# Performance work log

Hardware: AMD Instinct MI355X
Metric: run time of the kernel (lower is better)

## Reference

```python
import jax, jax.numpy as jnp
import numpy as np

N = 200000   # nodes
E = 600000   # edges
D = 128      # input_channels
H = 128      # hidden_channels
EPS = 1e-5   # BatchNorm1d eps


def setup_inputs() -> dict:
    key = jax.random.key(0)
    ks = jax.random.split(key, 6)
    x = jax.random.normal(ks[0], (N, D), dtype=jnp.float32)
    edge_index = jax.random.randint(ks[1], (2, E), 0, N)
    a1 = jnp.full((1,), 0.25, dtype=jnp.float32)   # PReLU init
    gamma = jnp.ones((D,), dtype=jnp.float32)
    beta = jnp.zeros((D,), dtype=jnp.float32)
    W1 = jax.random.normal(ks[2], (D, H), dtype=jnp.float32) / np.float32(np.sqrt(D))
    b1 = jnp.zeros((H,), dtype=jnp.float32)
    a2 = jnp.full((1,), 0.25, dtype=jnp.float32)
    W2 = jax.random.normal(ks[3], (H, D), dtype=jnp.float32) / np.float32(np.sqrt(H))
    b2 = jnp.zeros((D,), dtype=jnp.float32)
    return dict(x=x, edge_index=edge_index, a1=a1, gamma=gamma, beta=beta,
                W1=W1, b1=b1, a2=a2, W2=W2, b2=b2)


def _prelu(x, a):
    return jnp.where(x >= 0, x, a[0] * x)


def _batchnorm(x, gamma, beta):
    # training-mode BatchNorm1d: batch mean, biased variance
    mean = jnp.mean(x, axis=0)
    var = jnp.mean(jnp.square(x - mean), axis=0)
    return (x - mean) * jax.lax.rsqrt(var + EPS) * gamma + beta


def _gcn_conv(x, W, b, src, dst, n):
    # PyG GCNConv: add self-loops, symmetric normalization D^-1/2 (A+I) D^-1/2
    h = x @ W                                            # [n, out]
    deg = jnp.ones((n,), h.dtype).at[dst].add(1.0)       # degree incl. self-loop
    dinv = jax.lax.rsqrt(deg)
    coef = (dinv[src] * dinv[dst])[:, None]              # [E, 1]
    msg = h[src] * coef                                  # gather  [E, out]
    out = jax.ops.segment_sum(msg, dst, num_segments=n)  # scatter [n, out]
    out = out + h * (1.0 / deg)[:, None]                 # self-loop term
    return out + b


def reference(x, edge_index, a1, gamma, beta, W1, b1, a2, W2, b2):
    src, dst = edge_index[0], edge_index[1]
    n = x.shape[0]
    h = _prelu(x, a1)
    h = _batchnorm(h, gamma, beta)
    h = _gcn_conv(h, W1, b1, src, dst, n)
    h = _prelu(h, a2)
    h = _gcn_conv(h, W2, b2, src, dst, n)
    return h
```

## Files before the change

kernel.cpp:

```cpp
#include <hip/hip_runtime.h>

#define NN 200000
#define NE 600000
#define DD 128
#define GT 1563

constexpr float BN_EPS = 1e-5f;

typedef unsigned short u16;
typedef short bf16x8 __attribute__((ext_vector_type(8)));
typedef float f32x4  __attribute__((ext_vector_type(4)));
typedef float f32x2  __attribute__((ext_vector_type(2)));


__global__ void k_zero(int* __restrict__ cnt, float* __restrict__ ssum, float* __restrict__ ssq) {
  int i = blockIdx.x*256 + threadIdx.x;
  if (i < NN) cnt[i] = 0;
  if (i < DD) { ssum[i] = 0.f; ssq[i] = 0.f; }
}

__global__ void k_count(const int* __restrict__ ei, int* __restrict__ cnt) {
  int e = blockIdx.x*256 + threadIdx.x;
  if (e < NE) atomicAdd(&cnt[ei[NE + e]], 1);
}

__global__ void k_stats(const float* __restrict__ x, const float* __restrict__ a1p,
                        float* __restrict__ ssum, float* __restrict__ ssq) {
  __shared__ float s1[8][128], s2[8][128];
  const int c4 = (threadIdx.x & 31) * 4;
  const int rg = threadIdx.x >> 5;
  float a1 = *a1p;
  float acc1[4] = {0.f,0.f,0.f,0.f}, acc2[4] = {0.f,0.f,0.f,0.f};
  const int stride = gridDim.x * 8;
  for (int r = blockIdx.x*8 + rg; r < NN; r += stride) {
    float4 v = *(const float4*)(x + (size_t)r*DD + c4);
    float vv[4] = {v.x, v.y, v.z, v.w};
    #pragma unroll
    for (int i = 0; i < 4; ++i) {
      float u = vv[i];
      u = (u >= 0.f) ? u : a1*u;
      acc1[i] += u; acc2[i] += u*u;
    }
  }
  *(float4*)&s1[rg][c4] = make_float4(acc1[0], acc1[1], acc1[2], acc1[3]);
  *(float4*)&s2[rg][c4] = make_float4(acc2[0], acc2[1], acc2[2], acc2[3]);
  __syncthreads();
  if (threadIdx.x < 128) {
    int col = threadIdx.x;
    float t1 = 0.f, t2 = 0.f;
    #pragma unroll
    for (int g = 0; g < 8; ++g) { t1 += s1[g][col]; t2 += s2[g][col]; }
    atomicAdd(&ssum[col], t1);
    atomicAdd(&ssq [col], t2);
  }
}

__global__ void k_bn_tw1(const float* __restrict__ ssum, const float* __restrict__ ssq,
                         const float* __restrict__ gamma, const float* __restrict__ beta,
                         const float* __restrict__ W1,
                         float* __restrict__ sarr, float* __restrict__ tarr,
                         float* __restrict__ tw1) {
  __shared__ float ts[128];
  int j = threadIdx.x;
  float mean = ssum[j] * (1.f/NN);
  float var  = ssq[j] * (1.f/NN) - mean*mean;
  float s = gamma[j] * rsqrtf(var + BN_EPS);
  float t = beta[j] - mean*s;
  sarr[j] = s; tarr[j] = t; ts[j] = t;
  __syncthreads();
  float acc = 0.f;
  #pragma unroll 8
  for (int k = 0; k < 128; ++k) acc += ts[k] * W1[k*DD + j];
  tw1[j] = acc;
}

__global__ void k_wprep(const float* __restrict__ W, const float* __restrict__ s,
                        u16* __restrict__ hi, u16* __restrict__ lo) {
  int idx = blockIdx.x*256 + threadIdx.x;
  int j = idx >> 7, k = idx & 127;
  float v = W[(size_t)k*DD + j];
  if (s) v *= s[k];
  unsigned hb = __float_as_uint(v) & 0xffff0000u;
  float r = v - __uint_as_float(hb);
  hi[idx] = (u16)(hb >> 16);
  lo[idx] = (u16)(__float_as_uint(r) >> 16);
}


__global__ void k_scan1(const int* __restrict__ cnt, int* __restrict__ rp, int* __restrict__ bsums) {
  __shared__ int sm[256];
  int tid = threadIdx.x;
  int base = blockIdx.x*1024 + tid*4;
  int4 v = make_int4(0,0,0,0);
  if (base + 3 < NN) v = *(const int4*)(cnt + base);
  else {
    if (base   < NN) v.x = cnt[base];
    if (base+1 < NN) v.y = cnt[base+1];
    if (base+2 < NN) v.z = cnt[base+2];
    if (base+3 < NN) v.w = cnt[base+3];
  }
  int p1 = v.x, p2 = p1 + v.y, p3 = p2 + v.z, tsum = p3 + v.w;
  sm[tid] = tsum; __syncthreads();
  for (int off = 1; off < 256; off <<= 1) {
    int t = (tid >= off) ? sm[tid - off] : 0; __syncthreads();
    sm[tid] += t; __syncthreads();
  }
  int inc = sm[tid];
  int excl = inc - tsum;
  if (base   < NN) rp[base]   = excl;
  if (base+1 < NN) rp[base+1] = excl + p1;
  if (base+2 < NN) rp[base+2] = excl + p2;
  if (base+3 < NN) rp[base+3] = excl + p3;
  if (tid == 255) bsums[blockIdx.x] = inc;
}

__global__ void k_scan2(int* __restrict__ bsums, int nb) {
  __shared__ int sm[256];
  int tid = threadIdx.x;
  int v = (tid < nb) ? bsums[tid] : 0;
  sm[tid] = v; __syncthreads();
  for (int off = 1; off < 256; off <<= 1) {
    int t = (tid >= off) ? sm[tid - off] : 0; __syncthreads();
    sm[tid] += t; __syncthreads();
  }
  if (tid < nb) bsums[tid] = sm[tid] - v;
}

__global__ void k_scan3(int* __restrict__ rp, const int* __restrict__ bsums,
                        int* __restrict__ cur, const int* __restrict__ cnt,
                        float* __restrict__ dinv) {
  int i = blockIdx.x*256 + threadIdx.x;
  if (i < NN) {
    int val = rp[i] + bsums[i >> 10];
    rp[i] = val; cur[i] = val;
    dinv[i] = rsqrtf((float)(cnt[i] + 1));
  }
  if (i == 0) rp[NN] = NE;
}

__global__ void k_fill(const int* __restrict__ ei, const float* __restrict__ dinv,
                       int* __restrict__ cur, int2* __restrict__ pairs) {
  int e = blockIdx.x*256 + threadIdx.x;
  if (e < NE) {
    int s = ei[e], d = ei[NE + e];
    int pos = atomicAdd(&cur[d], 1);
    float cf = dinv[s] * dinv[d];
    pairs[pos] = make_int2(s, __float_as_int(cf));
  }
}


template<bool FUSE, bool ADDROW>
__global__ __launch_bounds__(256)
void k_gemm(const float* __restrict__ A,
            const u16* __restrict__ wt_hi, const u16* __restrict__ wt_lo,
            float* __restrict__ C,
            const float* __restrict__ tw1, const float* __restrict__ a1p)
{
  __shared__ u16 Bh[128][136];
  __shared__ u16 Bl[128][136];
  const int tid = threadIdx.x;

  #pragma unroll
  for (int i = 0; i < 8; ++i) {
    int c = tid + i*256;
    int row = c >> 4, slot = c & 15;
    *(uint4*)&Bh[row][slot*8] = ((const uint4*)wt_hi)[c];
    *(uint4*)&Bl[row][slot*8] = ((const uint4*)wt_lo)[c];
  }

  float a1v = 0.f;
  if constexpr (FUSE) a1v = *a1p;

  const int lane = tid & 63;
  const int wv   = tid >> 6;
  const int lr   = lane & 15;
  const int lk   = lane >> 4;
  const int r0   = blockIdx.x*128 + wv*32;

  f32x4 acc[2][8];
  #pragma unroll
  for (int s = 0; s < 2; ++s)
    #pragma unroll
    for (int j = 0; j < 8; ++j) acc[s][j] = (f32x4){0.f,0.f,0.f,0.f};

  __syncthreads();

  #pragma unroll
  for (int kc = 0; kc < 4; ++kc) {
    bf16x8 ah[2], al[2];
    #pragma unroll
    for (int s = 0; s < 2; ++s) {
      int r = r0 + s*16 + lr; r = (r < NN) ? r : (NN-1);
      const float* ap = A + (size_t)r*DD + kc*32 + lk*8;
      float4 v0 = *(const float4*)ap;
      float4 v1 = *(const float4*)(ap + 4);
      float vv[8] = {v0.x,v0.y,v0.z,v0.w,v1.x,v1.y,v1.z,v1.w};
      #pragma unroll
      for (int e = 0; e < 8; ++e) {
        float v = vv[e];
        if constexpr (FUSE) v = (v >= 0.f) ? v : a1v*v;
        unsigned hb = __float_as_uint(v) & 0xffff0000u;
        float rres = v - __uint_as_float(hb);
        ah[s][e] = (short)(hb >> 16);
        al[s][e] = (short)(__float_as_uint(rres) >> 16);
      }
    }
    #pragma unroll
    for (int j = 0; j < 8; ++j) {
      int wrow = j*16 + lr;
      bf16x8 bh = *(const bf16x8*)&Bh[wrow][kc*32 + lk*8];
      bf16x8 bl = *(const bf16x8*)&Bl[wrow][kc*32 + lk*8];
      #pragma unroll
      for (int s = 0; s < 2; ++s) {
        acc[s][j] = __builtin_amdgcn_mfma_f32_16x16x32_bf16(ah[s], bh, acc[s][j], 0, 0, 0);
        acc[s][j] = __builtin_amdgcn_mfma_f32_16x16x32_bf16(ah[s], bl, acc[s][j], 0, 0, 0);
        acc[s][j] = __builtin_amdgcn_mfma_f32_16x16x32_bf16(al[s], bh, acc[s][j], 0, 0, 0);
      }
    }
  }

  float tw[8];
  #pragma unroll
  for (int j = 0; j < 8; ++j) tw[j] = 0.f;
  if constexpr (ADDROW) {
    #pragma unroll
    for (int j = 0; j < 8; ++j) tw[j] = tw1[j*16 + lr];
  }

  #pragma unroll
  for (int s = 0; s < 2; ++s) {
    #pragma unroll
    for (int g = 0; g < 4; ++g) {
      int row = r0 + s*16 + lk*4 + g;
      if (row < NN) {
        float* cp = C + (size_t)row*DD + lr;
        #pragma unroll
        for (int j = 0; j < 8; ++j) cp[j*16] = acc[s][j][g] + tw[j];
      }
    }
  }
}


template<bool PRELU>
__global__ __launch_bounds__(256)
void k_agg(const float* __restrict__ h, const int* __restrict__ rp,
           const int2* __restrict__ pairs,
           const float* __restrict__ bias, const float* __restrict__ a2p,
           float* __restrict__ out)
{
  const int wave = threadIdx.x >> 6;
  const int lane = threadIdx.x & 63;
  const int nb = (blockIdx.x*4 + wave) * 8;
  if (nb >= NN) return;
  const float2* h2 = (const float2*)h;
  f32x2* o2 = (f32x2*)out;

  int rv = 0;
  if (lane < 9) rv = rp[nb + lane];
  int beg[8], cnt8[8];
  #pragma unroll
  for (int i = 0; i < 8; ++i) {
    int b0 = __builtin_amdgcn_readfirstlane(__shfl(rv, i));
    int b1 = __builtin_amdgcn_readfirstlane(__shfl(rv, i+1));
    beg[i] = b0; cnt8[i] = b1 - b0;
  }

  float2 b = ((const float2*)bias)[lane];
  float a2 = 1.f;
  if constexpr (PRELU) a2 = *a2p;

  float2 acc[8];
  #pragma unroll
  for (int i = 0; i < 8; ++i) {
    float2 self = h2[(size_t)(nb+i)*64 + lane];
    float sc = 1.f / (float)(cnt8[i] + 1);
    acc[i].x = sc*self.x + b.x;
    acc[i].y = sc*self.y + b.y;
  }

  int maxc = 0;
  #pragma unroll
  for (int i = 0; i < 8; ++i) maxc = max(maxc, cnt8[i]);

  for (int c = 0; c < maxc; ++c) {
    int2 p[8];
    #pragma unroll
    for (int i = 0; i < 8; ++i)
      if (c < cnt8[i]) p[i] = pairs[beg[i] + c];
    #pragma unroll
    for (int i = 0; i < 8; ++i)
      if (c < cnt8[i]) {
        float2 g = h2[(size_t)p[i].x*64 + lane];
        float cf = __int_as_float(p[i].y);
        acc[i].x += cf*g.x; acc[i].y += cf*g.y;
      }
  }

  #pragma unroll
  for (int i = 0; i < 8; ++i) {
    float ax = acc[i].x, ay = acc[i].y;
    if constexpr (PRELU) {
      ax = (ax >= 0.f) ? ax : a2*ax;
      ay = (ay >= 0.f) ? ay : a2*ay;
    }
    f32x2 o; o[0] = ax; o[1] = ay;
    __builtin_nontemporal_store(o, &o2[(size_t)(nb+i)*64 + lane]);
  }
}


extern "C" void kernel_launch(void* const* d_in, const int* in_sizes, int n_in,
                              void* d_out, int out_size, void* d_ws, size_t ws_size,
                              hipStream_t stream) {
  const float* x     = (const float*)d_in[0];
  const int*   ei    = (const int*)  d_in[1];
  const float* a1    = (const float*)d_in[2];
  const float* gamma = (const float*)d_in[3];
  const float* beta  = (const float*)d_in[4];
  const float* W1    = (const float*)d_in[5];
  const float* b1    = (const float*)d_in[6];
  const float* a2    = (const float*)d_in[7];
  const float* W2    = (const float*)d_in[8];
  const float* b2    = (const float*)d_in[9];
  float* out = (float*)d_out;

  char* w = (char*)d_ws;
  auto alloc = [&](size_t bytes) { char* p = w; w += (bytes + 255) & ~(size_t)255; return p; };
  float* hbuf  = (float*)alloc((size_t)NN*DD*4);
  float* dinv  = (float*)alloc((size_t)NN*4);
  int*   cnt   = (int*)  alloc((size_t)NN*4);
  int*   rp    = (int*)  alloc((size_t)(NN+1)*4);
  int*   cur   = (int*)  alloc((size_t)NN*4);
  int2*  pairs = (int2*) alloc((size_t)NE*8);
  int*   bsums = (int*)  alloc(256*4);
  float* ssum  = (float*)alloc(128*4);
  float* ssq   = (float*)alloc(128*4);
  float* sarr  = (float*)alloc(128*4);
  float* tarr  = (float*)alloc(128*4);
  float* tw1   = (float*)alloc(128*4);
  u16*   w1h   = (u16*)  alloc(128*128*2);
  u16*   w1l   = (u16*)  alloc(128*128*2);
  u16*   w2h   = (u16*)  alloc(128*128*2);
  u16*   w2l   = (u16*)  alloc(128*128*2);

  const int nblkN = (NN + 255)/256;
  const int nblkE = (NE + 255)/256;
  const int nblkA = NN/32;

  k_zero  <<<nblkN, 256, 0, stream>>>(cnt, ssum, ssq);
  k_count <<<nblkE, 256, 0, stream>>>(ei, cnt);
  k_stats <<<1024,  256, 0, stream>>>(x, a1, ssum, ssq);
  k_bn_tw1<<<1,     128, 0, stream>>>(ssum, ssq, gamma, beta, W1, sarr, tarr, tw1);
  k_wprep <<<64,    256, 0, stream>>>(W2, nullptr, w2h, w2l);
  k_wprep <<<64,    256, 0, stream>>>(W1, sarr,    w1h, w1l);
  k_scan1 <<<196,   256, 0, stream>>>(cnt, rp, bsums);
  k_scan2 <<<1,     256, 0, stream>>>(bsums, 196);
  k_scan3 <<<nblkN, 256, 0, stream>>>(rp, bsums, cur, cnt, dinv);
  k_fill  <<<nblkE, 256, 0, stream>>>(ei, dinv, cur, pairs);

  k_gemm<true,  true ><<<GT, 256, 0, stream>>>(x,   w1h, w1l, hbuf, tw1, a1);
  k_agg <true >        <<<nblkA, 256, 0, stream>>>(hbuf, rp, pairs, b1, a2, out);
  k_gemm<false, false><<<GT, 256, 0, stream>>>(out, w2h, w2l, hbuf, nullptr, nullptr);
  k_agg <false>        <<<nblkA, 256, 0, stream>>>(hbuf, rp, pairs, b2, nullptr, out);
}
```

Before: 515.9 us.

## Fuse first aggregation, PReLU and second GEMM into one kernel

Adds a kernel that aggregates neighbors for 32 nodes per block, applies bias and PReLU, splits the result into bf16 hi/lo parts in shared memory, and immediately multiplies by W2 with MFMA, writing the second-layer features to a new buffer. This removes one full N×128 fp32 write and read round-trip plus a separate GEMM launch. It needs an extra N×128 workspace buffer and falls back to the old path if the workspace is too small. W2 fragments are read straight from global memory in every block rather than staged.

After: 503.5 us. 2.4% less time.

```diff
diff --git a/kernel.cpp b/kernel.cpp
--- a/kernel.cpp
+++ b/kernel.cpp
@@ -240,6 +240,116 @@
       }
     }
   }
+}
+
+
+__global__ __launch_bounds__(256)
+void k_fagg(const float* __restrict__ h, const int* __restrict__ rp,
+            const int2* __restrict__ pairs,
+            const u16* __restrict__ w2h, const u16* __restrict__ w2l,
+            const float* __restrict__ b1, const float* __restrict__ a2p,
+            float* __restrict__ h2)
+{
+  __shared__ u16 Ghi[32][136];
+  __shared__ u16 Glo[32][136];
+  const int wave = threadIdx.x >> 6;
+  const int lane = threadIdx.x & 63;
+  const int nbB  = blockIdx.x * 32;
+  const int nb   = nbB + wave*8;
+  const float2* hv = (const float2*)h;
+
+  int rv = 0;
+  if (lane < 9) rv = rp[nb + lane];
+  int beg[8], cnt8[8];
+  #pragma unroll
+  for (int i = 0; i < 8; ++i) {
+    int b0 = __builtin_amdgcn_readfirstlane(__shfl(rv, i));
+    int b1v = __builtin_amdgcn_readfirstlane(__shfl(rv, i+1));
+    beg[i] = b0; cnt8[i] = b1v - b0;
+  }
+
+  float2 b = ((const float2*)b1)[lane];
+  float2 acc[8];
+  #pragma unroll
+  for (int i = 0; i < 8; ++i) {
+    float2 self = hv[(size_t)(nb+i)*64 + lane];
+    float sc = 1.f / (float)(cnt8[i] + 1);
+    acc[i].x = sc*self.x + b.x;
+    acc[i].y = sc*self.y + b.y;
+  }
+
+  int maxc = 0;
+  #pragma unroll
+  for (int i = 0; i < 8; ++i) maxc = max(maxc, cnt8[i]);
+
+  for (int c = 0; c < maxc; ++c) {
+    int2 p[8];
+    #pragma unroll
+    for (int i = 0; i < 8; ++i)
+      if (c < cnt8[i]) p[i] = pairs[beg[i] + c];
+    #pragma unroll
+    for (int i = 0; i < 8; ++i)
+      if (c < cnt8[i]) {
+        float2 g = hv[(size_t)p[i].x*64 + lane];
+        float cf = __int_as_float(p[i].y);
+        acc[i].x += cf*g.x; acc[i].y += cf*g.y;
+      }
+  }
+
+  float a2 = *a2p;
+  #pragma unroll
+  for (int i = 0; i < 8; ++i) {
+    float ax = acc[i].x, ay = acc[i].y;
+    ax = (ax >= 0.f) ? ax : a2*ax;
+    ay = (ay >= 0.f) ? ay : a2*ay;
+    unsigned hx = __float_as_uint(ax) & 0xffff0000u;
+    unsigned hy = __float_as_uint(ay) & 0xffff0000u;
+    float rx = ax - __uint_as_float(hx);
+    float ry = ay - __uint_as_float(hy);
+    unsigned hiw = (hx >> 16) | hy;
+    unsigned low = (__float_as_uint(rx) >> 16) | (__float_as_uint(ry) & 0xffff0000u);
+    int row = wave*8 + i;
+    *(unsigned*)&Ghi[row][lane*2] = hiw;
+    *(unsigned*)&Glo[row][lane*2] = low;
+  }
+  __syncthreads();
+
+  const int lr = lane & 15, lk = lane >> 4;
+  f32x4 dacc[2][2];
+  #pragma unroll
+  for (int s = 0; s < 2; ++s)
+    #pragma unroll
+    for (int t = 0; t < 2; ++t) dacc[s][t] = (f32x4){0.f,0.f,0.f,0.f};
+
+  #pragma unroll
+  for (int kc = 0; kc < 4; ++kc) {
+    bf16x8 ah0 = *(const bf16x8*)&Ghi[lr]   [kc*32 + lk*8];
+    bf16x8 al0 = *(const bf16x8*)&Glo[lr]   [kc*32 + lk*8];
+    bf16x8 ah1 = *(const bf16x8*)&Ghi[16+lr][kc*32 + lk*8];
+    bf16x8 al1 = *(const bf16x8*)&Glo[16+lr][kc*32 + lk*8];
+    #pragma unroll
+    for (int t = 0; t < 2; ++t) {
+      int wrow = wave*32 + t*16 + lr;
+      bf16x8 bh = *(const bf16x8*)(w2h + (size_t)wrow*DD + kc*32 + lk*8);
+      bf16x8 bl = *(const bf16x8*)(w2l + (size_t)wrow*DD + kc*32 + lk*8);
+      dacc[0][t] = __builtin_amdgcn_mfma_f32_16x16x32_bf16(ah0, bh, dacc[0][t], 0, 0, 0);
+      dacc[0][t] = __builtin_amdgcn_mfma_f32_16x16x32_bf16(ah0, bl, dacc[0][t], 0, 0, 0);
+      dacc[0][t] = __builtin_amdgcn_mfma_f32_16x16x32_bf16(al0, bh, dacc[0][t], 0, 0, 0);
+      dacc[1][t] = __builtin_amdgcn_mfma_f32_16x16x32_bf16(ah1, bh, dacc[1][t], 0, 0, 0);
+      dacc[1][t] = __builtin_amdgcn_mfma_f32_16x16x32_bf16(ah1, bl, dacc[1][t], 0, 0, 0);
+      dacc[1][t] = __builtin_amdgcn_mfma_f32_16x16x32_bf16(al1, bh, dacc[1][t], 0, 0, 0);
+    }
+  }
+
+  #pragma unroll
+  for (int s = 0; s < 2; ++s)
+    #pragma unroll
+    for (int t = 0; t < 2; ++t)
+      #pragma unroll
+      for (int g = 0; g < 4; ++g) {
+        int row = nbB + s*16 + lk*4 + g;
+        h2[(size_t)row*DD + wave*32 + t*16 + lr] = dacc[s][t][g];
+      }
 }
 
 
@@ -344,10 +454,13 @@
   u16*   w1l   = (u16*)  alloc(128*128*2);
   u16*   w2h   = (u16*)  alloc(128*128*2);
   u16*   w2l   = (u16*)  alloc(128*128*2);
+  float* hbuf2 = (float*)alloc((size_t)NN*DD*4);
+  const bool fused = ((size_t)(w - (char*)d_ws) <= ws_size);
 
   const int nblkN = (NN + 255)/256;
   const int nblkE = (NE + 255)/256;
   const int nblkA = NN/32;
+  const int nblkF = NN/32;
 
   k_zero  <<<nblkN, 256, 0, stream>>>(cnt, ssum, ssq);
   k_count <<<nblkE, 256, 0, stream>>>(ei, cnt);
@@ -360,8 +473,13 @@
   k_scan3 <<<nblkN, 256, 0, stream>>>(rp, bsums, cur, cnt, dinv);
   k_fill  <<<nblkE, 256, 0, stream>>>(ei, dinv, cur, pairs);
 
-  k_gemm<true,  true ><<<GT, 256, 0, stream>>>(x,   w1h, w1l, hbuf, tw1, a1);
-  k_agg <true >        <<<nblkA, 256, 0, stream>>>(hbuf, rp, pairs, b1, a2, out);
-  k_gemm<false, false><<<GT, 256, 0, stream>>>(out, w2h, w2l, hbuf, nullptr, nullptr);
-  k_agg <false>        <<<nblkA, 256, 0, stream>>>(hbuf, rp, pairs, b2, nullptr, out);
-}
+  k_gemm<true, true><<<GT, 256, 0, stream>>>(x, w1h, w1l, hbuf, tw1, a1);
+  if (fused) {
+    k_fagg<<<nblkF, 256, 0, stream>>>(hbuf, rp, pairs, w2h, w2l, b1, a2, hbuf2);
+    k_agg<false><<<nblkA, 256, 0, stream>>>(hbuf2, rp, pairs, b2, nullptr, out);
+  } else {
+    k_agg<true >         <<<nblkA, 256, 0, stream>>>(hbuf, rp, pairs, b1, a2, out);
+    k_gemm<false, false><<<GT, 256, 0, stream>>>(out, w2h, w2l, hbuf, nullptr, nullptr);
+    k_agg<false>         <<<nblkA, 256, 0, stream>>>(hbuf, rp, pairs, b2, nullptr, out);
+  }
+}
```
